# Performance work log

Measured on AMD Instinct MI355X. Metric: run time of the kernel, lower is better.

## Reference

```python
import jax, jax.numpy as jnp
import numpy as np

EMBED_DIM = 1024
NUM_HEADS = 16
HEAD_DIM = EMBED_DIM // NUM_HEADS
B, T = 8, 1024


def setup_inputs() -> dict:
    key = jax.random.key(0)
    ks = jax.random.split(key, 8)
    s = EMBED_DIM ** -0.5
    return {
        "query": jax.random.normal(ks[0], (B, T, EMBED_DIM), jnp.float32),
        "key": jax.random.normal(ks[1], (B, T, EMBED_DIM), jnp.float32),
        "value": jax.random.normal(ks[2], (B, T, EMBED_DIM), jnp.float32),
        "key_padding_mask": jnp.zeros((B, T), dtype=bool),
        "attn_mask": jax.random.normal(ks[3], (T, T), jnp.float32) * 0.02,
        "in_proj_weight": jax.random.normal(ks[4], (3 * EMBED_DIM, EMBED_DIM), jnp.float32) * s,
        "in_proj_bias": jax.random.normal(ks[5], (3 * EMBED_DIM,), jnp.float32) * 0.02,
        "out_proj_weight": jax.random.normal(ks[6], (EMBED_DIM, EMBED_DIM), jnp.float32) * s,
        "out_proj_bias": jax.random.normal(ks[7], (EMBED_DIM,), jnp.float32) * 0.02,
    }


def reference(query, key, value, key_padding_mask, attn_mask,
              in_proj_weight, in_proj_bias, out_proj_weight, out_proj_bias):
    E, H, Dh = EMBED_DIM, NUM_HEADS, HEAD_DIM
    scale = Dh ** -0.5
    w_q, w_k, w_v = in_proj_weight[:E], in_proj_weight[E:2 * E], in_proj_weight[2 * E:]
    b_q, b_k, b_v = in_proj_bias[:E], in_proj_bias[E:2 * E], in_proj_bias[2 * E:]

    b, t_q, _ = query.shape
    t_k = key.shape[1]
    # projections: F.linear(x, W, b) = x @ W.T + b
    q = (query @ w_q.T + b_q).reshape(b, t_q, H, Dh).transpose(0, 2, 1, 3)
    k = (key @ w_k.T + b_k).reshape(b, t_k, H, Dh).transpose(0, 2, 1, 3)
    v = (value @ w_v.T + b_v).reshape(b, t_k, H, Dh).transpose(0, 2, 1, 3)

    scores = jnp.einsum('bhqd,bhkd->bhqk', q, k) * scale  # [B,H,Tq,Tk]
    scores = jnp.where(key_padding_mask[:, None, None, :], -jnp.inf, scores)
    scores = scores + attn_mask  # broadcast [Tq,Tk] over batch/heads
    attn = jax.nn.softmax(scores, axis=-1)
    out = jnp.einsum('bhqk,bhkd->bhqd', attn, v)
    out = out.transpose(0, 2, 1, 3).reshape(b, t_q, E)
    return out @ out_proj_weight.T + out_proj_bias
```

## Files before the change

### kernel.cpp

```cpp
#include <hip/hip_runtime.h>
#include <cstdint>
#include <cstddef>

#define E_DIM   1024
#define NHEADS  16
#define DHEAD   64
#define BATCH   8
#define SEQ     1024
#define MROWS   (BATCH*SEQ)

#define LOG2E 1.44269504f

typedef __bf16 bf16;
typedef __attribute__((ext_vector_type(8))) __bf16 bf16x8;
typedef __attribute__((ext_vector_type(4))) __bf16 bf16x4;
typedef __attribute__((ext_vector_type(4))) float f32x4;

typedef const __attribute__((address_space(1))) unsigned int gu32;
typedef __attribute__((address_space(3))) unsigned int lu32;

__global__ __launch_bounds__(256)
void split_kernel(const float* __restrict__ src, bf16* __restrict__ hi,
                  bf16* __restrict__ lo, int n4)
{
    int i = blockIdx.x * 256 + threadIdx.x;
    if (i >= n4) return;
    float4 x = ((const float4*)src)[i];
    bf16x4 h, l;
    h[0] = (bf16)x.x; l[0] = (bf16)(x.x - (float)h[0]);
    h[1] = (bf16)x.y; l[1] = (bf16)(x.y - (float)h[1]);
    h[2] = (bf16)x.z; l[2] = (bf16)(x.z - (float)h[2]);
    h[3] = (bf16)x.w; l[3] = (bf16)(x.w - (float)h[3]);
    ((bf16x4*)hi)[i] = h;
    ((bf16x4*)lo)[i] = l;
}

__global__ __launch_bounds__(256)
void cvt_bf16_kernel(const float* __restrict__ src, bf16* __restrict__ dst,
                     float scale, int n4)
{
    int i = blockIdx.x * 256 + threadIdx.x;
    if (i >= n4) return;
    float4 x = ((const float4*)src)[i];
    bf16x4 h;
    h[0] = (bf16)(x.x * scale); h[1] = (bf16)(x.y * scale);
    h[2] = (bf16)(x.z * scale); h[3] = (bf16)(x.w * scale);
    ((bf16x4*)dst)[i] = h;
}

__global__ __launch_bounds__(512)
void gemm_nt_mfma(const bf16* __restrict__ Ahi, const bf16* __restrict__ Alo,
                  const bf16* __restrict__ Whi, const bf16* __restrict__ Wlo,
                  const float* __restrict__ bias,
                  float* __restrict__ outF, bf16* __restrict__ outHi,
                  int M, int N, int K, int mode)
{
    __shared__ bf16 Ahs[128 * 32];
    __shared__ bf16 Als[128 * 32];
    __shared__ bf16 Whs[128 * 32];
    __shared__ bf16 Wls[128 * 32];

    const int tid  = threadIdx.x;
    const int lane = tid & 63;
    const int wid  = tid >> 6;
    const int wm = (wid >> 1) * 32;
    const int wn = (wid & 1) * 64;
    const int fr = lane & 15;
    const int fk = (lane >> 4) * 8;

    const int mBase = blockIdx.y * 128;
    const int nBase = blockIdx.x * 128;

    const int rowA0 = tid >> 2;
    const int colA0 = (tid & 3) * 8;

    f32x4 acc[2][4];
#pragma unroll
    for (int i = 0; i < 2; ++i)
#pragma unroll
        for (int j = 0; j < 4; ++j) acc[i][j] = (f32x4){0.f, 0.f, 0.f, 0.f};

#pragma unroll 1
    for (int k0 = 0; k0 < K; k0 += 32) {
        const size_t ga0 = (size_t)(mBase + rowA0) * K + k0 + colA0;
        const size_t gw0 = (size_t)(nBase + rowA0) * K + k0 + colA0;
        __builtin_amdgcn_global_load_lds((gu32*)(Ahi + ga0), (lu32*)&Ahs[wid * 512], 16, 0, 0);
        __builtin_amdgcn_global_load_lds((gu32*)(Alo + ga0), (lu32*)&Als[wid * 512], 16, 0, 0);
        __builtin_amdgcn_global_load_lds((gu32*)(Whi + gw0), (lu32*)&Whs[wid * 512], 16, 0, 0);
        __builtin_amdgcn_global_load_lds((gu32*)(Wlo + gw0), (lu32*)&Wls[wid * 512], 16, 0, 0);
        __syncthreads();

        bf16x8 afh[2], afl[2], bfh[4], bfl[4];
#pragma unroll
        for (int am = 0; am < 2; ++am) {
            afh[am] = *(const bf16x8*)&Ahs[(wm + am * 16 + fr) * 32 + fk];
            afl[am] = *(const bf16x8*)&Als[(wm + am * 16 + fr) * 32 + fk];
        }
#pragma unroll
        for (int bn = 0; bn < 4; ++bn) {
            bfh[bn] = *(const bf16x8*)&Whs[(wn + bn * 16 + fr) * 32 + fk];
            bfl[bn] = *(const bf16x8*)&Wls[(wn + bn * 16 + fr) * 32 + fk];
        }
#pragma unroll
        for (int am = 0; am < 2; ++am)
#pragma unroll
            for (int bn = 0; bn < 4; ++bn) {
                acc[am][bn] = __builtin_amdgcn_mfma_f32_16x16x32_bf16(afh[am], bfh[bn], acc[am][bn], 0, 0, 0);
                acc[am][bn] = __builtin_amdgcn_mfma_f32_16x16x32_bf16(afh[am], bfl[bn], acc[am][bn], 0, 0, 0);
                acc[am][bn] = __builtin_amdgcn_mfma_f32_16x16x32_bf16(afl[am], bfh[bn], acc[am][bn], 0, 0, 0);
            }
        __syncthreads();
    }

    const int drow = (lane >> 4) * 4;
    const int dcol = lane & 15;
#pragma unroll
    for (int bn = 0; bn < 4; ++bn) {
        const int col = nBase + wn + bn * 16 + dcol;
        const float bv = bias[col];
#pragma unroll
        for (int am = 0; am < 2; ++am) {
#pragma unroll
            for (int r = 0; r < 4; ++r) {
                const int row = mBase + wm + am * 16 + drow + r;
                const float v = acc[am][bn][r] + bv;
                if (mode == 0) {
                    outF[(size_t)row * N + col] = v;
                } else {
                    const int b = row >> 10, t = row & 1023;
                    const int h = col >> 6,  d = col & 63;
                    size_t idx;
                    if (mode == 1)
                        idx = (((size_t)(b * NHEADS + h)) * SEQ + t) * DHEAD + d;
                    else
                        idx = (((size_t)(b * NHEADS + h)) * DHEAD + d) * SEQ + t;
                    outHi[idx] = (bf16)v;
                }
            }
        }
    }
}

__global__ __launch_bounds__(256)
void attn_mfma_kernel(const bf16* __restrict__ qkv,
                      const bf16* __restrict__ mask_bf,
                      const unsigned char* __restrict__ kpad,
                      bf16* __restrict__ ctx_hi, bf16* __restrict__ ctx_lo)
{
    __shared__ bf16 Ks [2][4096];
    __shared__ bf16 Vts[2][4096];
    __shared__ bf16 Pn[4][1024];

    const int tid  = threadIdx.x;
    const int lane = tid & 63;
    const int wid  = tid >> 6;
    const int c16  = lane & 15;
    const int quad = lane >> 4;

    const int bh = blockIdx.x;
    const int qt = blockIdx.y;
    const int b = bh >> 4, h = bh & 15;

    const size_t seg = (size_t)MROWS * E_DIM;
    const size_t headoff = (size_t)bh * SEQ * DHEAD;
    const bf16* Q_g  = qkv + headoff;
    const bf16* K_g  = qkv + seg + headoff;
    const bf16* Vt_g = qkv + 2 * seg + headoff;

    const int qglob = qt * 64 + wid * 16 + c16;

    bf16x8 qf[2];
#pragma unroll
    for (int ks = 0; ks < 2; ++ks)
        qf[ks] = *(const bf16x8*)&Q_g[(size_t)qglob * DHEAD + quad * 8 + ks * 32];

    float m_i = -1e30f, l_i = 0.f;
    f32x4 oacc[4];
#pragma unroll
    for (int dt = 0; dt < 4; ++dt) oacc[dt] = (f32x4){0.f, 0.f, 0.f, 0.f};

    const int row0 = tid >> 3,         c0 = (tid & 7) ^ (row0 & 7);
    const int row1 = (tid + 256) >> 3, c1 = ((tid + 256) & 7) ^ (row1 & 7);

    auto stage = [&](int kt, int bi) {
        const int ktb = kt * 64;
        const size_t k0 = (size_t)(ktb + row0) * DHEAD + c0 * 8;
        const size_t k1 = (size_t)(ktb + row1) * DHEAD + c1 * 8;
        const size_t v0 = (size_t)row0 * SEQ + ktb + c0 * 8;
        const size_t v1 = (size_t)row1 * SEQ + ktb + c1 * 8;
        __builtin_amdgcn_global_load_lds((gu32*)(K_g + k0),  (lu32*)&Ks [bi][wid * 512],        16, 0, 0);
        __builtin_amdgcn_global_load_lds((gu32*)(K_g + k1),  (lu32*)&Ks [bi][2048 + wid * 512], 16, 0, 0);
        __builtin_amdgcn_global_load_lds((gu32*)(Vt_g + v0), (lu32*)&Vts[bi][wid * 512],        16, 0, 0);
        __builtin_amdgcn_global_load_lds((gu32*)(Vt_g + v1), (lu32*)&Vts[bi][2048 + wid * 512], 16, 0, 0);
    };

    stage(0, 0);
    __syncthreads();

    const int pxor = (c16 & 7) << 3;
    const size_t kpb = (size_t)b * SEQ + quad * 4;

#pragma unroll 1
    for (int kt = 0; kt < 16; ++kt) {
        const int cur = kt & 1;
        const int ktb = kt * 64;

        bf16x4 mvh[4];
        uchar4 kp4[4];
#pragma unroll
        for (int st = 0; st < 4; ++st) {
            mvh[st] = *(const bf16x4*)&mask_bf[(size_t)qglob * SEQ + ktb + st * 16 + quad * 4];
            kp4[st] = *(const uchar4*)&kpad[kpb + ktb + st * 16];
        }

        if (kt < 15) stage(kt + 1, cur ^ 1);

        f32x4 sacc[4];
#pragma unroll
        for (int st = 0; st < 4; ++st) sacc[st] = (f32x4){0.f, 0.f, 0.f, 0.f};
#pragma unroll
        for (int st = 0; st < 4; ++st) {
            const int row = st * 16 + c16;
            const int sw  = row & 7;
#pragma unroll
            for (int ks = 0; ks < 2; ++ks) {
                const int cp = ((quad + ks * 4) ^ sw);
                bf16x8 kh = *(const bf16x8*)&Ks[cur][(row * 8 + cp) * 8];
                sacc[st] = __builtin_amdgcn_mfma_f32_16x16x32_bf16(kh, qf[ks], sacc[st], 0, 0, 0);
            }
        }

        float s[16];
#pragma unroll
        for (int st = 0; st < 4; ++st) {
#pragma unroll
            for (int r = 0; r < 4; ++r) {
                float sv = fmaf(sacc[st][r], 0.125f * LOG2E, (float)mvh[st][r]);
                const unsigned char kp = (r == 0) ? kp4[st].x : (r == 1) ? kp4[st].y
                                       : (r == 2) ? kp4[st].z : kp4[st].w;
                if (kp) sv = -2e30f;
                s[st * 4 + r] = sv;
            }
        }
        float t8[8];
#pragma unroll
        for (int i = 0; i < 8; ++i) t8[i] = fmaxf(s[i], s[i + 8]);
#pragma unroll
        for (int i = 0; i < 4; ++i) t8[i] = fmaxf(t8[i], t8[i + 4]);
        float tm = fmaxf(fmaxf(t8[0], t8[1]), fmaxf(t8[2], t8[3]));
        tm = fmaxf(tm, __shfl_xor(tm, 16, 64));
        tm = fmaxf(tm, __shfl_xor(tm, 32, 64));

        if (!__all(tm <= m_i + 11.5416f)) {
            const float mnew  = fmaxf(m_i, tm);
            const float alpha = __builtin_amdgcn_exp2f(m_i - mnew);
            l_i *= alpha;
#pragma unroll
            for (int dt = 0; dt < 4; ++dt)
#pragma unroll
                for (int r = 0; r < 4; ++r) oacc[dt][r] *= alpha;
            m_i = mnew;
        }

        float p[16];
#pragma unroll
        for (int i = 0; i < 16; ++i) p[i] = __builtin_amdgcn_exp2f(s[i] - m_i);
        float u8[8];
#pragma unroll
        for (int i = 0; i < 8; ++i) u8[i] = p[i] + p[i + 8];
#pragma unroll
        for (int i = 0; i < 4; ++i) u8[i] += u8[i + 4];
        float ps = (u8[0] + u8[1]) + (u8[2] + u8[3]);
        ps += __shfl_xor(ps, 16, 64);
        ps += __shfl_xor(ps, 32, 64);
        l_i += ps;

#pragma unroll
        for (int st = 0; st < 4; ++st) {
            bf16x4 ph;
#pragma unroll
            for (int r = 0; r < 4; ++r) ph[r] = (bf16)p[st * 4 + r];
            *(bf16x4*)&Pn[wid][c16 * 64 + ((st * 16 + quad * 4) ^ pxor)] = ph;
        }
        bf16x8 pf[2];
#pragma unroll
        for (int ks = 0; ks < 2; ++ks)
            pf[ks] = *(const bf16x8*)&Pn[wid][c16 * 64 + ((ks * 32 + quad * 8) ^ pxor)];

#pragma unroll
        for (int dt = 0; dt < 4; ++dt) {
            const int row = dt * 16 + c16;
            const int sw  = row & 7;
#pragma unroll
            for (int ks = 0; ks < 2; ++ks) {
                const int cp = ((quad + ks * 4) ^ sw);
                bf16x8 vh = *(const bf16x8*)&Vts[cur][(row * 8 + cp) * 8];
                oacc[dt] = __builtin_amdgcn_mfma_f32_16x16x32_bf16(vh, pf[ks], oacc[dt], 0, 0, 0);
            }
        }

        __syncthreads();
    }

    const float invl = 1.0f / l_i;
#pragma unroll
    for (int dt = 0; dt < 4; ++dt) {
        bf16x4 oh, ol;
#pragma unroll
        for (int r = 0; r < 4; ++r) {
            float v = oacc[dt][r] * invl;
            oh[r] = (bf16)v;
            ol[r] = (bf16)(v - (float)oh[r]);
        }
        size_t idx = ((size_t)b * SEQ + qglob) * E_DIM + h * DHEAD + dt * 16 + quad * 4;
        *(bf16x4*)&ctx_hi[idx] = oh;
        *(bf16x4*)&ctx_lo[idx] = ol;
    }
}

extern "C" void kernel_launch(void* const* d_in, const int* in_sizes, int n_in,
                              void* d_out, int out_size, void* d_ws, size_t ws_size,
                              hipStream_t stream)
{
    const float* inputs[3] = { (const float*)d_in[0], (const float*)d_in[1],
                               (const float*)d_in[2] };
    const unsigned char* kpad = (const unsigned char*)d_in[3];
    const float* attn_mask = (const float*)d_in[4];
    const float* w_in  = (const float*)d_in[5];
    const float* b_in  = (const float*)d_in[6];
    const float* w_out = (const float*)d_in[7];
    const float* b_out = (const float*)d_in[8];
    float* out = (float*)d_out;

    char* ws = (char*)d_ws;
    const size_t MB = 1024 * 1024;
    bf16* bufA_hi  = (bf16*)(ws + 0 * MB);
    bf16* bufA_lo  = (bf16*)(ws + 16 * MB);
    bf16* w_in_hi  = (bf16*)(ws + 32 * MB);
    bf16* w_in_lo  = (bf16*)(ws + 38 * MB);
    bf16* w_out_hi = (bf16*)(ws + 44 * MB);
    bf16* w_out_lo = (bf16*)(ws + 46 * MB);
    bf16* qkv      = (bf16*)(ws + 48 * MB);
    bf16* mask_bf  = (bf16*)(ws + 96 * MB);
    bf16* ctx_hi   = (bf16*)(ws + 0 * MB);
    bf16* ctx_lo   = (bf16*)(ws + 16 * MB);

    const size_t seg = (size_t)MROWS * E_DIM;

    split_kernel<<<(3 * E_DIM * E_DIM / 4 + 255) / 256, 256, 0, stream>>>(
        w_in, w_in_hi, w_in_lo, 3 * E_DIM * E_DIM / 4);
    split_kernel<<<(E_DIM * E_DIM / 4 + 255) / 256, 256, 0, stream>>>(
        w_out, w_out_hi, w_out_lo, E_DIM * E_DIM / 4);
    cvt_bf16_kernel<<<(SEQ * SEQ / 4 + 255) / 256, 256, 0, stream>>>(
        attn_mask, mask_bf, LOG2E, SEQ * SEQ / 4);

    for (int z = 0; z < 3; ++z) {
        split_kernel<<<(int)(seg / 4 / 256), 256, 0, stream>>>(
            inputs[z], bufA_hi, bufA_lo, (int)(seg / 4));
        gemm_nt_mfma<<<dim3(E_DIM / 128, MROWS / 128), 512, 0, stream>>>(
            bufA_hi, bufA_lo,
            w_in_hi + (size_t)z * E_DIM * E_DIM, w_in_lo + (size_t)z * E_DIM * E_DIM,
            b_in + z * E_DIM,
            nullptr, qkv + (size_t)z * seg,
            MROWS, E_DIM, E_DIM, (z == 2) ? 2 : 1);
    }

    attn_mfma_kernel<<<dim3(BATCH * NHEADS, SEQ / 64), 256, 0, stream>>>(
        qkv, mask_bf, kpad, ctx_hi, ctx_lo);

    gemm_nt_mfma<<<dim3(E_DIM / 128, MROWS / 128), 512, 0, stream>>>(
        ctx_hi, ctx_lo, w_out_hi, w_out_lo, b_out,
        out, nullptr, MROWS, E_DIM, E_DIM, 0);
}
```

Measured before the change: 519.2 us.

## Double-buffer GEMM LDS tiles, keep mask in fp32, skip padding when absent

The split-bf16 GEMM now double-buffers its LDS tiles, issuing the next K-slice's global-to-LDS loads before waiting on the current ones with explicit vmcnt waits and raw barriers, so load latency can overlap the MFMA work. The bias is hoisted into registers before the main loop. The attention mask is kept in fp32 rather than rounded to bf16, which improves accuracy but doubles mask read traffic. The key-padding test becomes a wave-wide any() check that skips the per-element masking when no keys are padded. Doubling LDS use may lower GEMM occupancy.

```diff
diff --git a/kernel.cpp b/kernel.cpp
--- a/kernel.cpp
+++ b/kernel.cpp
@@ -36,16 +36,14 @@
 }
 
 __global__ __launch_bounds__(256)
-void cvt_bf16_kernel(const float* __restrict__ src, bf16* __restrict__ dst,
-                     float scale, int n4)
+void scale_f32_kernel(const float* __restrict__ src, float* __restrict__ dst,
+                      float scale, int n4)
 {
     int i = blockIdx.x * 256 + threadIdx.x;
     if (i >= n4) return;
     float4 x = ((const float4*)src)[i];
-    bf16x4 h;
-    h[0] = (bf16)(x.x * scale); h[1] = (bf16)(x.y * scale);
-    h[2] = (bf16)(x.z * scale); h[3] = (bf16)(x.w * scale);
-    ((bf16x4*)dst)[i] = h;
+    x.x *= scale; x.y *= scale; x.z *= scale; x.w *= scale;
+    ((float4*)dst)[i] = x;
 }
 
 __global__ __launch_bounds__(512)
@@ -55,10 +53,10 @@
                   float* __restrict__ outF, bf16* __restrict__ outHi,
                   int M, int N, int K, int mode)
 {
-    __shared__ bf16 Ahs[128 * 32];
-    __shared__ bf16 Als[128 * 32];
-    __shared__ bf16 Whs[128 * 32];
-    __shared__ bf16 Wls[128 * 32];
+    __shared__ bf16 Ahs[2][128 * 32];
+    __shared__ bf16 Als[2][128 * 32];
+    __shared__ bf16 Whs[2][128 * 32];
+    __shared__ bf16 Wls[2][128 * 32];
 
     const int tid  = threadIdx.x;
     const int lane = tid & 63;
@@ -74,32 +72,56 @@
     const int rowA0 = tid >> 2;
     const int colA0 = (tid & 3) * 8;
 
+    const int dcol = lane & 15;
+    float bv[4];
+#pragma unroll
+    for (int bn = 0; bn < 4; ++bn)
+        bv[bn] = bias[nBase + wn + bn * 16 + dcol];
+
     f32x4 acc[2][4];
 #pragma unroll
     for (int i = 0; i < 2; ++i)
 #pragma unroll
         for (int j = 0; j < 4; ++j) acc[i][j] = (f32x4){0.f, 0.f, 0.f, 0.f};
 
-#pragma unroll 1
-    for (int k0 = 0; k0 < K; k0 += 32) {
+    auto stage = [&](int k0, int bi) {
         const size_t ga0 = (size_t)(mBase + rowA0) * K + k0 + colA0;
         const size_t gw0 = (size_t)(nBase + rowA0) * K + k0 + colA0;
-        __builtin_amdgcn_global_load_lds((gu32*)(Ahi + ga0), (lu32*)&Ahs[wid * 512], 16, 0, 0);
-        __builtin_amdgcn_global_load_lds((gu32*)(Alo + ga0), (lu32*)&Als[wid * 512], 16, 0, 0);
-        __builtin_amdgcn_global_load_lds((gu32*)(Whi + gw0), (lu32*)&Whs[wid * 512], 16, 0, 0);
-        __builtin_amdgcn_global_load_lds((gu32*)(Wlo + gw0), (lu32*)&Wls[wid * 512], 16, 0, 0);
-        __syncthreads();
+        __builtin_amdgcn_global_load_lds((gu32*)(Ahi + ga0), (lu32*)&Ahs[bi][wid * 512], 16, 0, 0);
+        __builtin_amdgcn_global_load_lds((gu32*)(Alo + ga0), (lu32*)&Als[bi][wid * 512], 16, 0, 0);
+        __builtin_amdgcn_global_load_lds((gu32*)(Whi + gw0), (lu32*)&Whs[bi][wid * 512], 16, 0, 0);
+        __builtin_amdgcn_global_load_lds((gu32*)(Wlo + gw0), (lu32*)&Wls[bi][wid * 512], 16, 0, 0);
+    };
+
+    stage(0, 0);
+
+    const int NIT = K >> 5;
+#pragma unroll 1
+    for (int it = 0; it < NIT; ++it) {
+        const int cur = it & 1;
+        if (it + 1 < NIT) {
+            stage((it + 1) << 5, cur ^ 1);
+            asm volatile("s_waitcnt vmcnt(4)" ::: "memory");
+        } else {
+            asm volatile("s_waitcnt vmcnt(0)" ::: "memory");
+        }
+        __builtin_amdgcn_s_barrier();
+
+        const bf16* As = Ahs[cur];
+        const bf16* Al = Als[cur];
+        const bf16* Ws = Whs[cur];
+        const bf16* Wl = Wls[cur];
 
         bf16x8 afh[2], afl[2], bfh[4], bfl[4];
 #pragma unroll
         for (int am = 0; am < 2; ++am) {
-            afh[am] = *(const bf16x8*)&Ahs[(wm + am * 16 + fr) * 32 + fk];
-            afl[am] = *(const bf16x8*)&Als[(wm + am * 16 + fr) * 32 + fk];
+            afh[am] = *(const bf16x8*)&As[(wm + am * 16 + fr) * 32 + fk];
+            afl[am] = *(const bf16x8*)&Al[(wm + am * 16 + fr) * 32 + fk];
         }
 #pragma unroll
         for (int bn = 0; bn < 4; ++bn) {
-            bfh[bn] = *(const bf16x8*)&Whs[(wn + bn * 16 + fr) * 32 + fk];
-            bfl[bn] = *(const bf16x8*)&Wls[(wn + bn * 16 + fr) * 32 + fk];
+            bfh[bn] = *(const bf16x8*)&Ws[(wn + bn * 16 + fr) * 32 + fk];
+            bfl[bn] = *(const bf16x8*)&Wl[(wn + bn * 16 + fr) * 32 + fk];
         }
 #pragma unroll
         for (int am = 0; am < 2; ++am)
@@ -109,21 +131,19 @@
                 acc[am][bn] = __builtin_amdgcn_mfma_f32_16x16x32_bf16(afh[am], bfl[bn], acc[am][bn], 0, 0, 0);
                 acc[am][bn] = __builtin_amdgcn_mfma_f32_16x16x32_bf16(afl[am], bfh[bn], acc[am][bn], 0, 0, 0);
             }
-        __syncthreads();
+        __builtin_amdgcn_s_barrier();
     }
 
     const int drow = (lane >> 4) * 4;
-    const int dcol = lane & 15;
 #pragma unroll
     for (int bn = 0; bn < 4; ++bn) {
         const int col = nBase + wn + bn * 16 + dcol;
-        const float bv = bias[col];
 #pragma unroll
         for (int am = 0; am < 2; ++am) {
 #pragma unroll
             for (int r = 0; r < 4; ++r) {
                 const int row = mBase + wm + am * 16 + drow + r;
-                const float v = acc[am][bn][r] + bv;
+                const float v = acc[am][bn][r] + bv[bn];
                 if (mode == 0) {
                     outF[(size_t)row * N + col] = v;
                 } else {
@@ -143,7 +163,7 @@
 
 __global__ __launch_bounds__(256)
 void attn_mfma_kernel(const bf16* __restrict__ qkv,
-                      const bf16* __restrict__ mask_bf,
+                      const float* __restrict__ mask_f,
                       const unsigned char* __restrict__ kpad,
                       bf16* __restrict__ ctx_hi, bf16* __restrict__ ctx_lo)
 {
@@ -205,12 +225,12 @@
         const int cur = kt & 1;
         const int ktb = kt * 64;
 
-        bf16x4 mvh[4];
-        uchar4 kp4[4];
+        float4 mvf[4];
+        unsigned kpu[4];
 #pragma unroll
         for (int st = 0; st < 4; ++st) {
-            mvh[st] = *(const bf16x4*)&mask_bf[(size_t)qglob * SEQ + ktb + st * 16 + quad * 4];
-            kp4[st] = *(const uchar4*)&kpad[kpb + ktb + st * 16];
+            mvf[st] = *(const float4*)&mask_f[(size_t)qglob * SEQ + ktb + st * 16 + quad * 4];
+            kpu[st] = *(const unsigned*)&kpad[kpb + ktb + st * 16];
         }
 
         if (kt < 15) stage(kt + 1, cur ^ 1);
@@ -235,12 +255,17 @@
         for (int st = 0; st < 4; ++st) {
 #pragma unroll
             for (int r = 0; r < 4; ++r) {
-                float sv = fmaf(sacc[st][r], 0.125f * LOG2E, (float)mvh[st][r]);
-                const unsigned char kp = (r == 0) ? kp4[st].x : (r == 1) ? kp4[st].y
-                                       : (r == 2) ? kp4[st].z : kp4[st].w;
-                if (kp) sv = -2e30f;
-                s[st * 4 + r] = sv;
-            }
+                const float mv = (r == 0) ? mvf[st].x : (r == 1) ? mvf[st].y
+                               : (r == 2) ? mvf[st].z : mvf[st].w;
+                s[st * 4 + r] = fmaf(sacc[st][r], 0.125f * LOG2E, mv);
+            }
+        }
+        if (__any((kpu[0] | kpu[1] | kpu[2] | kpu[3]) != 0u)) {
+#pragma unroll
+            for (int st = 0; st < 4; ++st)
+#pragma unroll
+                for (int r = 0; r < 4; ++r)
+                    if ((kpu[st] >> (r * 8)) & 0xff) s[st * 4 + r] = -2e30f;
         }
         float t8[8];
 #pragma unroll
@@ -334,16 +359,16 @@
 
     char* ws = (char*)d_ws;
     const size_t MB = 1024 * 1024;
-    bf16* bufA_hi  = (bf16*)(ws + 0 * MB);
-    bf16* bufA_lo  = (bf16*)(ws + 16 * MB);
-    bf16* w_in_hi  = (bf16*)(ws + 32 * MB);
-    bf16* w_in_lo  = (bf16*)(ws + 38 * MB);
-    bf16* w_out_hi = (bf16*)(ws + 44 * MB);
-    bf16* w_out_lo = (bf16*)(ws + 46 * MB);
-    bf16* qkv      = (bf16*)(ws + 48 * MB);
-    bf16* mask_bf  = (bf16*)(ws + 96 * MB);
-    bf16* ctx_hi   = (bf16*)(ws + 0 * MB);
-    bf16* ctx_lo   = (bf16*)(ws + 16 * MB);
+    bf16*  bufA_hi  = (bf16*)(ws + 0 * MB);
+    bf16*  bufA_lo  = (bf16*)(ws + 16 * MB);
+    bf16*  w_in_hi  = (bf16*)(ws + 32 * MB);
+    bf16*  w_in_lo  = (bf16*)(ws + 38 * MB);
+    bf16*  w_out_hi = (bf16*)(ws + 44 * MB);
+    bf16*  w_out_lo = (bf16*)(ws + 46 * MB);
+    bf16*  qkv      = (bf16*)(ws + 48 * MB);
+    float* mask_f   = (float*)(ws + 96 * MB);
+    bf16*  ctx_hi   = (bf16*)(ws + 0 * MB);
+    bf16*  ctx_lo   = (bf16*)(ws + 16 * MB);
 
     const size_t seg = (size_t)MROWS * E_DIM;
 
@@ -351,8 +376,8 @@
         w_in, w_in_hi, w_in_lo, 3 * E_DIM * E_DIM / 4);
     split_kernel<<<(E_DIM * E_DIM / 4 + 255) / 256, 256, 0, stream>>>(
         w_out, w_out_hi, w_out_lo, E_DIM * E_DIM / 4);
-    cvt_bf16_kernel<<<(SEQ * SEQ / 4 + 255) / 256, 256, 0, stream>>>(
-        attn_mask, mask_bf, LOG2E, SEQ * SEQ / 4);
+    scale_f32_kernel<<<(SEQ * SEQ / 4 + 255) / 256, 256, 0, stream>>>(
+        attn_mask, mask_f, LOG2E, SEQ * SEQ / 4);
 
     for (int z = 0; z < 3; ++z) {
         split_kernel<<<(int)(seg / 4 / 256), 256, 0, stream>>>(
@@ -366,7 +391,7 @@
     }
 
     attn_mfma_kernel<<<dim3(BATCH * NHEADS, SEQ / 64), 256, 0, stream>>>(
-        qkv, mask_bf, kpad, ctx_hi, ctx_lo);
+        qkv, mask_f, kpad, ctx_hi, ctx_lo);
 
     gemm_nt_mfma<<<dim3(E_DIM / 128, MROWS / 128), 512, 0, stream>>>(
         ctx_hi, ctx_lo, w_out_hi, w_out_lo, b_out,
```

Result: no change. 514.1 us (-1.0%).
